# Optimization experiments

Hardware: AMD Instinct MI355X
Metric: run time of the kernel (lower is better)

Reference implementation:

```python
import jax, jax.numpy as jnp
import numpy as np

EPS = 1e-12  # matches torch F.normalize eps


def _l2norm(v, axis):
    return v / jnp.maximum(jnp.linalg.norm(v, axis=axis, keepdims=True), EPS)


def setup_inputs() -> dict:
    key = jax.random.key(0)
    k1, k2, k3 = jax.random.split(key, 3)
    B, C, H, W, K = 32, 512, 40, 40, 64
    x = jax.random.normal(k1, (B, C, H, W), dtype=jnp.float32)
    centroids = jax.random.uniform(k2, (K, C), dtype=jnp.float32)  # torch.rand init
    assign_w = jax.random.normal(k3, (K, C), dtype=jnp.float32)    # 1x1 conv weight, no bias
    return {"x": x, "centroids": centroids, "assign_w": assign_w}


def reference(x, centroids, assign_w):
    # x: [B, C, H, W]; centroids/assign_w: [K, C]
    B, C, H, W = x.shape
    x = _l2norm(x, axis=1)                      # channel-wise L2 normalize
    xf = x.reshape(B, C, H * W)                 # [B, C, N]
    # 1x1 conv == per-pixel matmul with [K, C] weight
    logits = jnp.einsum('kc,bcn->bkn', assign_w, xf)
    a = jax.nn.softmax(logits, axis=1)          # softmax over clusters, [B, K, N]
    # vlad[b,k,c] = sum_n a[b,k,n] * (x[b,c,n] - centroid[k,c])
    #            = (a @ x^T)[b,k,c] - centroid[k,c] * sum_n a[b,k,n]
    vlad = jnp.einsum('bkn,bcn->bkc', a, xf) - a.sum(axis=-1)[..., None] * centroids[None]
    vlad = _l2norm(vlad, axis=2)                # intra-normalization per cluster
    vlad = vlad.reshape(B, -1)                  # [B, K*C]
    return _l2norm(vlad, axis=1)                # global L2 normalize
```

## Files before the change

kernel.cpp:

```cpp
#include <hip/hip_runtime.h>
#include <math.h>

#define BB   32
#define CC   512
#define NPIX 1600
#define KK   64
#define NT   25
#define EPSF 1e-12f

typedef __attribute__((ext_vector_type(8))) short bf16x8;
typedef __attribute__((ext_vector_type(4))) float f32x4;
#define MFMA16 __builtin_amdgcn_mfma_f32_16x16x32_bf16

__device__ __forceinline__ ushort f2bf(float f) {
    union { float f; uint u; } v; v.f = f;
    uint r = v.u + 0x7FFFu + ((v.u >> 16) & 1u);
    return (ushort)(r >> 16);
}

__global__ __launch_bounds__(256) void k_gemm1m(const float* __restrict__ x,
                                                const float* __restrict__ w,
                                                ushort* __restrict__ a_t,
                                                float* __restrict__ asum_p) {
    int tile = blockIdx.x, b = blockIdx.y;
    int n0 = tile * 64;
    __shared__ __align__(16) ushort Xs[2][64 * 32];
    __shared__ __align__(16) ushort Wsh[2][64 * 32];
    __shared__ __align__(16) float red[16 * 64];
    __shared__ __align__(16) float asw[4 * 64];
    __shared__ __align__(16) float ivs[64];
    int t = threadIdx.x;
    int lane = t & 63, wv = t >> 6;
    int sc2 = (t & 15) * 2;
    int sn4 = (t >> 4) * 4;
    int wk  = t >> 2;
    int wc8 = (t & 3) * 8;
    const float* xb = x + (size_t)b * CC * NPIX + n0;
    f32x4 acc[4] = {};
    float ss[4] = {0.f, 0.f, 0.f, 0.f};

    float4 xa, xc, wa, wc2;
    xa  = *(const float4*)&xb[(size_t)sc2 * NPIX + sn4];
    xc  = *(const float4*)&xb[(size_t)(sc2 + 1) * NPIX + sn4];
    wa  = *(const float4*)&w[(size_t)wk * CC + wc8];
    wc2 = *(const float4*)&w[(size_t)wk * CC + wc8 + 4];
    {
        uint* XU = (uint*)Xs[0]; uint* WU = (uint*)Wsh[0];
        float va[4] = {xa.x, xa.y, xa.z, xa.w};
        float vc[4] = {xc.x, xc.y, xc.z, xc.w};
#pragma unroll
        for (int j = 0; j < 4; ++j) {
            ss[j] += va[j] * va[j] + vc[j] * vc[j];
            int row = sn4 + j;
            int gp = ((t & 15) >> 2) ^ ((row >> 1) & 3);
            XU[row * 16 + gp * 4 + (t & 3)] =
                (uint)f2bf(va[j]) | ((uint)f2bf(vc[j]) << 16);
        }
        uint4 wp;
        wp.x = (uint)f2bf(wa.x)  | ((uint)f2bf(wa.y)  << 16);
        wp.y = (uint)f2bf(wa.z)  | ((uint)f2bf(wa.w)  << 16);
        wp.z = (uint)f2bf(wc2.x) | ((uint)f2bf(wc2.y) << 16);
        wp.w = (uint)f2bf(wc2.z) | ((uint)f2bf(wc2.w) << 16);
        int gp = (t & 3) ^ ((wk >> 1) & 3);
        *(uint4*)&WU[wk * 16 + gp * 4] = wp;
    }
    __syncthreads();

    int cur = 0;
    for (int it = 0; it < 16; ++it) {
        bool pre = (it < 15);
        if (pre) {
            int c0 = (it + 1) * 32;
            xa  = *(const float4*)&xb[(size_t)(c0 + sc2) * NPIX + sn4];
            xc  = *(const float4*)&xb[(size_t)(c0 + sc2 + 1) * NPIX + sn4];
            wa  = *(const float4*)&w[(size_t)wk * CC + c0 + wc8];
            wc2 = *(const float4*)&w[(size_t)wk * CC + c0 + wc8 + 4];
        }
        {
            const ushort* Xc = Xs[cur];
            const ushort* Wc = Wsh[cur];
            int rn = wv * 16 + (lane & 15);
            int gB = (lane >> 4) ^ ((rn >> 1) & 3);
            bf16x8 bfr = *(const bf16x8*)&Xc[rn * 32 + gB * 8];
#pragma unroll
            for (int kf = 0; kf < 4; ++kf) {
                int rk = kf * 16 + (lane & 15);
                int gA = (lane >> 4) ^ ((rk >> 1) & 3);
                bf16x8 afr = *(const bf16x8*)&Wc[rk * 32 + gA * 8];
                acc[kf] = MFMA16(afr, bfr, acc[kf], 0, 0, 0);
            }
        }
        if (pre) {
            uint* XU = (uint*)Xs[cur ^ 1]; uint* WU = (uint*)Wsh[cur ^ 1];
            float va[4] = {xa.x, xa.y, xa.z, xa.w};
            float vc[4] = {xc.x, xc.y, xc.z, xc.w};
#pragma unroll
            for (int j = 0; j < 4; ++j) {
                ss[j] += va[j] * va[j] + vc[j] * vc[j];
                int row = sn4 + j;
                int gp = ((t & 15) >> 2) ^ ((row >> 1) & 3);
                XU[row * 16 + gp * 4 + (t & 3)] =
                    (uint)f2bf(va[j]) | ((uint)f2bf(vc[j]) << 16);
            }
            uint4 wp;
            wp.x = (uint)f2bf(wa.x)  | ((uint)f2bf(wa.y)  << 16);
            wp.y = (uint)f2bf(wa.z)  | ((uint)f2bf(wa.w)  << 16);
            wp.z = (uint)f2bf(wc2.x) | ((uint)f2bf(wc2.y) << 16);
            wp.w = (uint)f2bf(wc2.z) | ((uint)f2bf(wc2.w) << 16);
            int gp = (t & 3) ^ ((wk >> 1) & 3);
            *(uint4*)&WU[wk * 16 + gp * 4] = wp;
        }
        __syncthreads();
        cur ^= 1;
    }

#pragma unroll
    for (int j = 0; j < 4; ++j) red[(t & 15) * 64 + sn4 + j] = ss[j];
    __syncthreads();
    if (t < 64) {
        float s = 0.f;
#pragma unroll
        for (int i = 0; i < 16; ++i) s += red[i * 64 + t];
        ivs[t] = 1.f / fmaxf(sqrtf(s), EPSF);
    }
    __syncthreads();

    int nloc = wv * 16 + (lane & 15);
    float invl = ivs[nloc];

    float lv[4][4];
    float mm = -1e30f;
#pragma unroll
    for (int kf = 0; kf < 4; ++kf)
#pragma unroll
        for (int r = 0; r < 4; ++r) {
            lv[kf][r] = acc[kf][r] * invl;
            mm = fmaxf(mm, lv[kf][r]);
        }
    mm = fmaxf(mm, __shfl_xor(mm, 16));
    mm = fmaxf(mm, __shfl_xor(mm, 32));
    float ev[4][4], s = 0.f;
#pragma unroll
    for (int kf = 0; kf < 4; ++kf)
#pragma unroll
        for (int r = 0; r < 4; ++r) {
            ev[kf][r] = expf(lv[kf][r] - mm);
            s += ev[kf][r];
        }
    s += __shfl_xor(s, 16);
    s += __shfl_xor(s, 32);
    float sd = 1.f / s;

    float av[4][4];
#pragma unroll
    for (int kf = 0; kf < 4; ++kf)
#pragma unroll
        for (int r = 0; r < 4; ++r) av[kf][r] = ev[kf][r] * sd;
#pragma unroll
    for (int off = 1; off < 16; off <<= 1)
#pragma unroll
        for (int kf = 0; kf < 4; ++kf)
#pragma unroll
            for (int r = 0; r < 4; ++r) av[kf][r] += __shfl_xor(av[kf][r], off);
    if ((lane & 15) == 0) {
#pragma unroll
        for (int kf = 0; kf < 4; ++kf)
#pragma unroll
            for (int r = 0; r < 4; ++r)
                asw[wv * 64 + kf * 16 + (lane >> 4) * 4 + r] = av[kf][r];
    }

    ushort* ab = a_t + (size_t)b * KK * NPIX;
#pragma unroll
    for (int kf = 0; kf < 4; ++kf)
#pragma unroll
        for (int r = 0; r < 4; ++r) {
            int k = kf * 16 + (lane >> 4) * 4 + r;
            ab[(size_t)k * NPIX + n0 + nloc] = f2bf(ev[kf][r] * sd * invl);
        }
    __syncthreads();
    if (t < 64) {
        float a4 = asw[t] + asw[64 + t] + asw[128 + t] + asw[192 + t];
        asum_p[((size_t)b * KK + t) * NT + tile] = a4;
    }
}

__global__ __launch_bounds__(256) void k_vladm(const ushort* __restrict__ a_t,
                                               const float* __restrict__ x,
                                               float* __restrict__ part,
                                               int nchunk) {
    int c0 = blockIdx.x * 64;
    int s  = blockIdx.y;
    int b  = blockIdx.z;
    __shared__ __align__(16) ushort Ash[2][64 * 32];
    __shared__ __align__(16) ushort Xsh[2][64 * 32];
    int t = threadIdx.x;
    int lane = t & 63, wv = t >> 6;
    int sk  = t >> 2;
    int sn8 = (t & 3) * 8;
    const ushort* ab = a_t + (size_t)b * KK * NPIX;
    const float*  xb = x + (size_t)b * CC * NPIX;
    f32x4 acc[4] = {};
    int nbase = s * nchunk;
    int niters = nchunk / 32;

    uint4 ar; float4 x0, x1;
    ar = *(const uint4*)&ab[(size_t)sk * NPIX + nbase + sn8];
    x0 = *(const float4*)&xb[(size_t)(c0 + sk) * NPIX + nbase + sn8];
    x1 = *(const float4*)&xb[(size_t)(c0 + sk) * NPIX + nbase + sn8 + 4];
    {
        uint* AU = (uint*)Ash[0]; uint* XU = (uint*)Xsh[0];
        int gp = (t & 3) ^ ((sk >> 1) & 3);
        *(uint4*)&AU[sk * 16 + gp * 4] = ar;
        uint4 xp;
        xp.x = (uint)f2bf(x0.x) | ((uint)f2bf(x0.y) << 16);
        xp.y = (uint)f2bf(x0.z) | ((uint)f2bf(x0.w) << 16);
        xp.z = (uint)f2bf(x1.x) | ((uint)f2bf(x1.y) << 16);
        xp.w = (uint)f2bf(x1.z) | ((uint)f2bf(x1.w) << 16);
        *(uint4*)&XU[sk * 16 + gp * 4] = xp;
    }
    __syncthreads();

    int cur = 0;
    for (int it = 0; it < niters; ++it) {
        bool pre = (it + 1 < niters);
        if (pre) {
            int ng = nbase + (it + 1) * 32;
            ar = *(const uint4*)&ab[(size_t)sk * NPIX + ng + sn8];
            x0 = *(const float4*)&xb[(size_t)(c0 + sk) * NPIX + ng + sn8];
            x1 = *(const float4*)&xb[(size_t)(c0 + sk) * NPIX + ng + sn8 + 4];
        }
        {
            const ushort* Ac = Ash[cur];
            const ushort* Xc = Xsh[cur];
            int rc = wv * 16 + (lane & 15);
            int gB = (lane >> 4) ^ ((rc >> 1) & 3);
            bf16x8 bfr = *(const bf16x8*)&Xc[rc * 32 + gB * 8];
#pragma unroll
            for (int kf = 0; kf < 4; ++kf) {
                int rk = kf * 16 + (lane & 15);
                int gA = (lane >> 4) ^ ((rk >> 1) & 3);
                bf16x8 afr = *(const bf16x8*)&Ac[rk * 32 + gA * 8];
                acc[kf] = MFMA16(afr, bfr, acc[kf], 0, 0, 0);
            }
        }
        if (pre) {
            uint* AU = (uint*)Ash[cur ^ 1]; uint* XU = (uint*)Xsh[cur ^ 1];
            int gp = (t & 3) ^ ((sk >> 1) & 3);
            *(uint4*)&AU[sk * 16 + gp * 4] = ar;
            uint4 xp;
            xp.x = (uint)f2bf(x0.x) | ((uint)f2bf(x0.y) << 16);
            xp.y = (uint)f2bf(x0.z) | ((uint)f2bf(x0.w) << 16);
            xp.z = (uint)f2bf(x1.x) | ((uint)f2bf(x1.y) << 16);
            xp.w = (uint)f2bf(x1.z) | ((uint)f2bf(x1.w) << 16);
            *(uint4*)&XU[sk * 16 + gp * 4] = xp;
        }
        __syncthreads();
        cur ^= 1;
    }

#pragma unroll
    for (int kf = 0; kf < 4; ++kf)
#pragma unroll
        for (int r = 0; r < 4; ++r) {
            int k = kf * 16 + (lane >> 4) * 4 + r;
            int c = c0 + wv * 16 + (lane & 15);
            part[(((size_t)s * BB + b) * KK + k) * CC + c] = acc[kf][r];
        }
}

__global__ __launch_bounds__(256) void k_intra(const float* __restrict__ part, int ns,
                                               const float* __restrict__ asum_p,
                                               const float* __restrict__ cent,
                                               float* __restrict__ out,
                                               float* __restrict__ bsum) {
    int row = blockIdx.x;
    int b = row >> 6, k = row & 63;
    int t = threadIdx.x;
    float v0 = 0.f, v1 = 0.f;
    for (int s2 = 0; s2 < ns; ++s2) {
        const float* p = part + (((size_t)s2 * BB + b) * KK + k) * CC;
        v0 += p[t];
        v1 += p[t + 256];
    }
    float as = 0.f;
#pragma unroll
    for (int i = 0; i < NT; ++i) as += asum_p[(size_t)row * NT + i];
    v0 -= as * cent[k * CC + t];
    v1 -= as * cent[k * CC + t + 256];
    float ssq = v0 * v0 + v1 * v1;
#pragma unroll
    for (int off = 32; off; off >>= 1) ssq += __shfl_down(ssq, off, 64);
    __shared__ float red[4];
    __shared__ float s_inv;
    if ((t & 63) == 0) red[t >> 6] = ssq;
    __syncthreads();
    if (t == 0) {
        float sm = red[0] + red[1] + red[2] + red[3];
        float inv = 1.f / fmaxf(sqrtf(sm), EPSF);
        s_inv = inv;
        atomicAdd(&bsum[b], sm * inv * inv);
    }
    __syncthreads();
    float inv = s_inv;
    out[(size_t)row * CC + t]       = v0 * inv;
    out[(size_t)row * CC + t + 256] = v1 * inv;
}

__global__ __launch_bounds__(256) void k_scale(float* __restrict__ out,
                                               const float* __restrict__ bsum) {
    int idx = blockIdx.x * 256 + threadIdx.x;
    int b = idx >> 15;
    out[idx] *= 1.f / fmaxf(sqrtf(bsum[b]), EPSF);
}

extern "C" void kernel_launch(void* const* d_in, const int* in_sizes, int n_in,
                              void* d_out, int out_size, void* d_ws, size_t ws_size,
                              hipStream_t stream) {
    const float* x    = (const float*)d_in[0];
    const float* cent = (const float*)d_in[1];
    const float* w    = (const float*)d_in[2];
    float* out = (float*)d_out;

    char* wsb = (char*)d_ws;
    const size_t oa_at   = 0;
    const size_t oa_asum = oa_at + (size_t)BB * KK * NPIX * 2;
    const size_t oa_bsum = oa_asum + (size_t)BB * KK * NT * 4;
    const size_t oa_part = oa_bsum + 128;
    ushort* a_t   = (ushort*)(wsb + oa_at);
    float* asum_p = (float*)(wsb + oa_asum);
    float* bsum   = (float*)(wsb + oa_bsum);

    const size_t pbytes = (size_t)BB * KK * CC * 4;
    int ns = 0;
    const int cand[3] = {5, 2, 1};
    for (int i = 0; i < 3; ++i) {
        if (oa_part + (size_t)cand[i] * pbytes <= ws_size) { ns = cand[i]; break; }
    }
    float* part = (ns > 0) ? (float*)(wsb + oa_part) : out;
    if (ns == 0) ns = 1;
    int nchunk = NPIX / ns;

    hipMemsetAsync(bsum, 0, BB * sizeof(float), stream);

    k_gemm1m<<<dim3(NT, BB), 256, 0, stream>>>(x, w, a_t, asum_p);
    k_vladm <<<dim3(CC / 64, ns, BB), 256, 0, stream>>>(a_t, x, part, nchunk);
    k_intra <<<dim3(BB * KK), 256, 0, stream>>>(part, ns, asum_p, cent, out, bsum);
    k_scale <<<dim3((BB * KK * CC) / 256), 256, 0, stream>>>(out, bsum);
}
```

Measured before the change: 88.59 us.

## Load MFMA fragments directly from global memory, drop LDS staging, pre-convert weights to bf16

Both GEMM kernels stop staging tiles through double-buffered shared memory and instead load each lane's MFMA operand fragment straight from global memory, removing the per-iteration barriers and LDS traffic. A new small kernel converts the assignment weights to bf16 once per call, so the first GEMM reads packed bf16 weights directly. The per-pixel sum of squares now becomes a cross-lane shuffle instead of a shared-memory reduction. The cost is less coalesced global access: the first GEMM reads x with strided scalar loads, and fragments are re-read across waves without LDS reuse, relying on cache.

```diff
diff --git a/kernel.cpp b/kernel.cpp
--- a/kernel.cpp
+++ b/kernel.cpp
@@ -1,4 +1,5 @@
 #include <hip/hip_runtime.h>
+#include <hip/hip_bf16.h>
 #include <math.h>
 
 #define BB   32
@@ -13,120 +14,57 @@
 #define MFMA16 __builtin_amdgcn_mfma_f32_16x16x32_bf16
 
 __device__ __forceinline__ ushort f2bf(float f) {
-    union { float f; uint u; } v; v.f = f;
-    uint r = v.u + 0x7FFFu + ((v.u >> 16) & 1u);
-    return (ushort)(r >> 16);
+    __hip_bfloat16 h = __float2bfloat16(f);
+    return *reinterpret_cast<ushort*>(&h);
+}
+__device__ __forceinline__ uint pk2bf(float a, float b) {
+    return (uint)f2bf(a) | ((uint)f2bf(b) << 16);
+}
+
+__global__ __launch_bounds__(256) void k_wprep(const float* __restrict__ w,
+                                               ushort* __restrict__ wb) {
+    int i = blockIdx.x * 256 + threadIdx.x;
+    float2 v = *(const float2*)&w[(size_t)i * 2];
+    ((uint*)wb)[i] = pk2bf(v.x, v.y);
 }
 
 __global__ __launch_bounds__(256) void k_gemm1m(const float* __restrict__ x,
-                                                const float* __restrict__ w,
+                                                const ushort* __restrict__ wb,
                                                 ushort* __restrict__ a_t,
                                                 float* __restrict__ asum_p) {
     int tile = blockIdx.x, b = blockIdx.y;
     int n0 = tile * 64;
-    __shared__ __align__(16) ushort Xs[2][64 * 32];
-    __shared__ __align__(16) ushort Wsh[2][64 * 32];
-    __shared__ __align__(16) float red[16 * 64];
-    __shared__ __align__(16) float asw[4 * 64];
-    __shared__ __align__(16) float ivs[64];
-    int t = threadIdx.x;
-    int lane = t & 63, wv = t >> 6;
-    int sc2 = (t & 15) * 2;
-    int sn4 = (t >> 4) * 4;
-    int wk  = t >> 2;
-    int wc8 = (t & 3) * 8;
-    const float* xb = x + (size_t)b * CC * NPIX + n0;
+    int t = threadIdx.x, lane = t & 63, wv = t >> 6;
+    int nlo = lane & 15, khi = lane >> 4;
+    int rn = wv * 16 + nlo;
+    const float* xb = x + (size_t)b * CC * NPIX + n0 + rn;
+    __shared__ float asw[4 * 64];
     f32x4 acc[4] = {};
-    float ss[4] = {0.f, 0.f, 0.f, 0.f};
-
-    float4 xa, xc, wa, wc2;
-    xa  = *(const float4*)&xb[(size_t)sc2 * NPIX + sn4];
-    xc  = *(const float4*)&xb[(size_t)(sc2 + 1) * NPIX + sn4];
-    wa  = *(const float4*)&w[(size_t)wk * CC + wc8];
-    wc2 = *(const float4*)&w[(size_t)wk * CC + wc8 + 4];
-    {
-        uint* XU = (uint*)Xs[0]; uint* WU = (uint*)Wsh[0];
-        float va[4] = {xa.x, xa.y, xa.z, xa.w};
-        float vc[4] = {xc.x, xc.y, xc.z, xc.w};
-#pragma unroll
-        for (int j = 0; j < 4; ++j) {
-            ss[j] += va[j] * va[j] + vc[j] * vc[j];
-            int row = sn4 + j;
-            int gp = ((t & 15) >> 2) ^ ((row >> 1) & 3);
-            XU[row * 16 + gp * 4 + (t & 3)] =
-                (uint)f2bf(va[j]) | ((uint)f2bf(vc[j]) << 16);
-        }
-        uint4 wp;
-        wp.x = (uint)f2bf(wa.x)  | ((uint)f2bf(wa.y)  << 16);
-        wp.y = (uint)f2bf(wa.z)  | ((uint)f2bf(wa.w)  << 16);
-        wp.z = (uint)f2bf(wc2.x) | ((uint)f2bf(wc2.y) << 16);
-        wp.w = (uint)f2bf(wc2.z) | ((uint)f2bf(wc2.w) << 16);
-        int gp = (t & 3) ^ ((wk >> 1) & 3);
-        *(uint4*)&WU[wk * 16 + gp * 4] = wp;
-    }
-    __syncthreads();
-
-    int cur = 0;
+    float ss = 0.f;
+
     for (int it = 0; it < 16; ++it) {
-        bool pre = (it < 15);
-        if (pre) {
-            int c0 = (it + 1) * 32;
-            xa  = *(const float4*)&xb[(size_t)(c0 + sc2) * NPIX + sn4];
-            xc  = *(const float4*)&xb[(size_t)(c0 + sc2 + 1) * NPIX + sn4];
-            wa  = *(const float4*)&w[(size_t)wk * CC + c0 + wc8];
-            wc2 = *(const float4*)&w[(size_t)wk * CC + c0 + wc8 + 4];
-        }
-        {
-            const ushort* Xc = Xs[cur];
-            const ushort* Wc = Wsh[cur];
-            int rn = wv * 16 + (lane & 15);
-            int gB = (lane >> 4) ^ ((rn >> 1) & 3);
-            bf16x8 bfr = *(const bf16x8*)&Xc[rn * 32 + gB * 8];
-#pragma unroll
-            for (int kf = 0; kf < 4; ++kf) {
-                int rk = kf * 16 + (lane & 15);
-                int gA = (lane >> 4) ^ ((rk >> 1) & 3);
-                bf16x8 afr = *(const bf16x8*)&Wc[rk * 32 + gA * 8];
-                acc[kf] = MFMA16(afr, bfr, acc[kf], 0, 0, 0);
-            }
-        }
-        if (pre) {
-            uint* XU = (uint*)Xs[cur ^ 1]; uint* WU = (uint*)Wsh[cur ^ 1];
-            float va[4] = {xa.x, xa.y, xa.z, xa.w};
-            float vc[4] = {xc.x, xc.y, xc.z, xc.w};
-#pragma unroll
-            for (int j = 0; j < 4; ++j) {
-                ss[j] += va[j] * va[j] + vc[j] * vc[j];
-                int row = sn4 + j;
-                int gp = ((t & 15) >> 2) ^ ((row >> 1) & 3);
-                XU[row * 16 + gp * 4 + (t & 3)] =
-                    (uint)f2bf(va[j]) | ((uint)f2bf(vc[j]) << 16);
-            }
-            uint4 wp;
-            wp.x = (uint)f2bf(wa.x)  | ((uint)f2bf(wa.y)  << 16);
-            wp.y = (uint)f2bf(wa.z)  | ((uint)f2bf(wa.w)  << 16);
-            wp.z = (uint)f2bf(wc2.x) | ((uint)f2bf(wc2.y) << 16);
-            wp.w = (uint)f2bf(wc2.z) | ((uint)f2bf(wc2.w) << 16);
-            int gp = (t & 3) ^ ((wk >> 1) & 3);
-            *(uint4*)&WU[wk * 16 + gp * 4] = wp;
-        }
-        __syncthreads();
-        cur ^= 1;
-    }
-
-#pragma unroll
-    for (int j = 0; j < 4; ++j) red[(t & 15) * 64 + sn4 + j] = ss[j];
-    __syncthreads();
-    if (t < 64) {
-        float s = 0.f;
-#pragma unroll
-        for (int i = 0; i < 16; ++i) s += red[i * 64 + t];
-        ivs[t] = 1.f / fmaxf(sqrtf(s), EPSF);
-    }
-    __syncthreads();
-
-    int nloc = wv * 16 + (lane & 15);
-    float invl = ivs[nloc];
+        int cbase = it * 32 + khi * 8;
+        float f[8];
+#pragma unroll
+        for (int j = 0; j < 8; ++j)
+            f[j] = xb[(size_t)(cbase + j) * NPIX];
+        uint4 bp;
+        bp.x = pk2bf(f[0], f[1]); bp.y = pk2bf(f[2], f[3]);
+        bp.z = pk2bf(f[4], f[5]); bp.w = pk2bf(f[6], f[7]);
+        bf16x8 bfr = *reinterpret_cast<bf16x8*>(&bp);
+#pragma unroll
+        for (int j = 0; j < 8; ++j) ss = fmaf(f[j], f[j], ss);
+#pragma unroll
+        for (int kf = 0; kf < 4; ++kf) {
+            int rk = kf * 16 + nlo;
+            bf16x8 afr = *(const bf16x8*)&wb[(size_t)rk * CC + cbase];
+            acc[kf] = MFMA16(afr, bfr, acc[kf], 0, 0, 0);
+        }
+    }
+
+    ss += __shfl_xor(ss, 16);
+    ss += __shfl_xor(ss, 32);
+    float invl = 1.f / fmaxf(sqrtf(ss), EPSF);
 
     float lv[4][4];
     float mm = -1e30f;
@@ -162,12 +100,12 @@
         for (int kf = 0; kf < 4; ++kf)
 #pragma unroll
             for (int r = 0; r < 4; ++r) av[kf][r] += __shfl_xor(av[kf][r], off);
-    if ((lane & 15) == 0) {
+    if (nlo == 0) {
 #pragma unroll
         for (int kf = 0; kf < 4; ++kf)
 #pragma unroll
             for (int r = 0; r < 4; ++r)
-                asw[wv * 64 + kf * 16 + (lane >> 4) * 4 + r] = av[kf][r];
+                asw[wv * 64 + kf * 16 + khi * 4 + r] = av[kf][r];
     }
 
     ushort* ab = a_t + (size_t)b * KK * NPIX;
@@ -175,8 +113,8 @@
     for (int kf = 0; kf < 4; ++kf)
 #pragma unroll
         for (int r = 0; r < 4; ++r) {
-            int k = kf * 16 + (lane >> 4) * 4 + r;
-            ab[(size_t)k * NPIX + n0 + nloc] = f2bf(ev[kf][r] * sd * invl);
+            int k = kf * 16 + khi * 4 + r;
+            ab[(size_t)k * NPIX + n0 + rn] = f2bf(ev[kf][r] * sd * invl);
         }
     __syncthreads();
     if (t < 64) {
@@ -192,80 +130,36 @@
     int c0 = blockIdx.x * 64;
     int s  = blockIdx.y;
     int b  = blockIdx.z;
-    __shared__ __align__(16) ushort Ash[2][64 * 32];
-    __shared__ __align__(16) ushort Xsh[2][64 * 32];
-    int t = threadIdx.x;
-    int lane = t & 63, wv = t >> 6;
-    int sk  = t >> 2;
-    int sn8 = (t & 3) * 8;
+    int t = threadIdx.x, lane = t & 63, wv = t >> 6;
+    int clo = lane & 15, nhi = lane >> 4;
+    int rc = wv * 16 + clo;
     const ushort* ab = a_t + (size_t)b * KK * NPIX;
-    const float*  xb = x + (size_t)b * CC * NPIX;
+    const float*  xr = x + (size_t)b * CC * NPIX + (size_t)(c0 + rc) * NPIX;
     f32x4 acc[4] = {};
-    int nbase = s * nchunk;
-    int niters = nchunk / 32;
-
-    uint4 ar; float4 x0, x1;
-    ar = *(const uint4*)&ab[(size_t)sk * NPIX + nbase + sn8];
-    x0 = *(const float4*)&xb[(size_t)(c0 + sk) * NPIX + nbase + sn8];
-    x1 = *(const float4*)&xb[(size_t)(c0 + sk) * NPIX + nbase + sn8 + 4];
-    {
-        uint* AU = (uint*)Ash[0]; uint* XU = (uint*)Xsh[0];
-        int gp = (t & 3) ^ ((sk >> 1) & 3);
-        *(uint4*)&AU[sk * 16 + gp * 4] = ar;
-        uint4 xp;
-        xp.x = (uint)f2bf(x0.x) | ((uint)f2bf(x0.y) << 16);
-        xp.y = (uint)f2bf(x0.z) | ((uint)f2bf(x0.w) << 16);
-        xp.z = (uint)f2bf(x1.x) | ((uint)f2bf(x1.y) << 16);
-        xp.w = (uint)f2bf(x1.z) | ((uint)f2bf(x1.w) << 16);
-        *(uint4*)&XU[sk * 16 + gp * 4] = xp;
-    }
-    __syncthreads();
-
-    int cur = 0;
+    int nbase = s * nchunk, niters = nchunk / 32;
+
     for (int it = 0; it < niters; ++it) {
-        bool pre = (it + 1 < niters);
-        if (pre) {
-            int ng = nbase + (it + 1) * 32;
-            ar = *(const uint4*)&ab[(size_t)sk * NPIX + ng + sn8];
-            x0 = *(const float4*)&xb[(size_t)(c0 + sk) * NPIX + ng + sn8];
-            x1 = *(const float4*)&xb[(size_t)(c0 + sk) * NPIX + ng + sn8 + 4];
-        }
-        {
-            const ushort* Ac = Ash[cur];
-            const ushort* Xc = Xsh[cur];
-            int rc = wv * 16 + (lane & 15);
-            int gB = (lane >> 4) ^ ((rc >> 1) & 3);
-            bf16x8 bfr = *(const bf16x8*)&Xc[rc * 32 + gB * 8];
-#pragma unroll
-            for (int kf = 0; kf < 4; ++kf) {
-                int rk = kf * 16 + (lane & 15);
-                int gA = (lane >> 4) ^ ((rk >> 1) & 3);
-                bf16x8 afr = *(const bf16x8*)&Ac[rk * 32 + gA * 8];
-                acc[kf] = MFMA16(afr, bfr, acc[kf], 0, 0, 0);
-            }
-        }
-        if (pre) {
-            uint* AU = (uint*)Ash[cur ^ 1]; uint* XU = (uint*)Xsh[cur ^ 1];
-            int gp = (t & 3) ^ ((sk >> 1) & 3);
-            *(uint4*)&AU[sk * 16 + gp * 4] = ar;
-            uint4 xp;
-            xp.x = (uint)f2bf(x0.x) | ((uint)f2bf(x0.y) << 16);
-            xp.y = (uint)f2bf(x0.z) | ((uint)f2bf(x0.w) << 16);
-            xp.z = (uint)f2bf(x1.x) | ((uint)f2bf(x1.y) << 16);
-            xp.w = (uint)f2bf(x1.z) | ((uint)f2bf(x1.w) << 16);
-            *(uint4*)&XU[sk * 16 + gp * 4] = xp;
-        }
-        __syncthreads();
-        cur ^= 1;
-    }
-
-#pragma unroll
-    for (int kf = 0; kf < 4; ++kf)
-#pragma unroll
-        for (int r = 0; r < 4; ++r) {
-            int k = kf * 16 + (lane >> 4) * 4 + r;
-            int c = c0 + wv * 16 + (lane & 15);
-            part[(((size_t)s * BB + b) * KK + k) * CC + c] = acc[kf][r];
+        int nb = nbase + it * 32 + nhi * 8;
+        float4 x0 = *(const float4*)&xr[nb];
+        float4 x1 = *(const float4*)&xr[nb + 4];
+        uint4 bp;
+        bp.x = pk2bf(x0.x, x0.y); bp.y = pk2bf(x0.z, x0.w);
+        bp.z = pk2bf(x1.x, x1.y); bp.w = pk2bf(x1.z, x1.w);
+        bf16x8 bfr = *reinterpret_cast<bf16x8*>(&bp);
+#pragma unroll
+        for (int kf = 0; kf < 4; ++kf) {
+            int rk = kf * 16 + clo;
+            bf16x8 afr = *(const bf16x8*)&ab[(size_t)rk * NPIX + nb];
+            acc[kf] = MFMA16(afr, bfr, acc[kf], 0, 0, 0);
+        }
+    }
+
+#pragma unroll
+    for (int kf = 0; kf < 4; ++kf)
+#pragma unroll
+        for (int r = 0; r < 4; ++r) {
+            int k = kf * 16 + nhi * 4 + r;
+            part[(((size_t)s * BB + b) * KK + k) * CC + c0 + rc] = acc[kf][r];
         }
 }
 
@@ -324,10 +218,12 @@
 
     char* wsb = (char*)d_ws;
     const size_t oa_at   = 0;
-    const size_t oa_asum = oa_at + (size_t)BB * KK * NPIX * 2;
+    const size_t oa_wb   = oa_at + (size_t)BB * KK * NPIX * 2;
+    const size_t oa_asum = oa_wb + (size_t)KK * CC * 2;
     const size_t oa_bsum = oa_asum + (size_t)BB * KK * NT * 4;
     const size_t oa_part = oa_bsum + 128;
     ushort* a_t   = (ushort*)(wsb + oa_at);
+    ushort* wb    = (ushort*)(wsb + oa_wb);
     float* asum_p = (float*)(wsb + oa_asum);
     float* bsum   = (float*)(wsb + oa_bsum);
 
@@ -343,7 +239,8 @@
 
     hipMemsetAsync(bsum, 0, BB * sizeof(float), stream);
 
-    k_gemm1m<<<dim3(NT, BB), 256, 0, stream>>>(x, w, a_t, asum_p);
+    k_wprep <<<dim3((KK * CC / 2) / 256), 256, 0, stream>>>(w, wb);
+    k_gemm1m<<<dim3(NT, BB), 256, 0, stream>>>(x, wb, a_t, asum_p);
     k_vladm <<<dim3(CC / 64, ns, BB), 256, 0, stream>>>(a_t, x, part, nchunk);
     k_intra <<<dim3(BB * KK), 256, 0, stream>>>(part, ns, asum_p, cent, out, bsum);
     k_scale <<<dim3((BB * KK * CC) / 256), 256, 0, stream>>>(out, bsum);
```

Result: slower. 112.9 us (+27.5%).
